# Optimization experiments

Hardware: AMD Instinct MI355X
Metric: run time of the kernel (lower is better)

## Reference

```python
import jax, jax.numpy as jnp
import numpy as np

N_HEAD = 16
NUM_GROUPS = 2


def setup_inputs() -> dict:
    key = jax.random.key(0)
    k1, k2, k3 = jax.random.split(key, 3)
    B, T, D = 4, 2048, 1024
    x = jax.random.normal(k1, (B, T, D), dtype=jnp.float32)
    W_attn = jax.random.normal(k2, (D, 3 * D), dtype=jnp.float32) * 0.02
    b_attn = jnp.zeros((3 * D,), dtype=jnp.float32)
    W_proj = jax.random.normal(k3, (D, D), dtype=jnp.float32) * 0.02
    b_proj = jnp.zeros((D,), dtype=jnp.float32)
    return {"x": x, "W_attn": W_attn, "b_attn": b_attn, "W_proj": W_proj, "b_proj": b_proj}


def _rope_tables(T, d_head):
    # thetas = 1000 ** (-2*arange(1, d/2+1)/d), repeat_interleave(2); positions start at 1
    half = d_head // 2
    thetas = 1000.0 ** (-2.0 * jnp.arange(1, half + 1, dtype=jnp.float32) / d_head)
    thetas = jnp.repeat(thetas, 2)                      # (d_head,)
    pos = jnp.arange(1, T + 1, dtype=jnp.float32)       # (T,)
    args = pos[:, None] * thetas[None, :]               # (T, d_head)
    return jnp.sin(args), jnp.cos(args)


def _apply_rope(x, sin, cos):
    # x: (B, H, T, d_head)
    x_odd = x[..., ::2]
    x_even = x[..., 1::2]
    x_sin = jnp.stack([-x_even, x_odd], axis=-1).reshape(x.shape)  # [-x1, x0, -x3, x2, ...]
    return x * cos + x_sin * sin


def reference(x, W_attn, b_attn, W_proj, b_proj):
    B, T, D = x.shape
    H = N_HEAD
    hd = D // H
    group_dim = D // NUM_GROUPS  # scale divisor; split degenerates to one group since group_dim >= hd

    qkv = x @ W_attn + b_attn                              # (B, T, 3D)
    q, k, v = jnp.split(qkv, 3, axis=-1)

    def split_heads(t):
        return t.reshape(B, T, H, hd).transpose(0, 2, 1, 3)  # (B, H, T, hd)

    q, k, v = split_heads(q), split_heads(k), split_heads(v)

    sin, cos = _rope_tables(T, hd)
    q = _apply_rope(q, sin, cos)
    k = _apply_rope(k, sin, cos)

    # NOTE: original forward never applies the causal mask (attn_mask=None) -> full softmax
    scores = jnp.einsum('bhqd,bhkd->bhqk', q, k) / jnp.sqrt(jnp.float32(group_dim))
    attn = jax.nn.softmax(scores, axis=-1)
    out = jnp.einsum('bhqk,bhkd->bhqd', attn, v)           # (B, H, T, hd)

    out = out.transpose(0, 2, 1, 3).reshape(B, T, D)       # merge heads
    return out @ W_proj + b_proj
```

## Files before the change

kernel.cpp:

```cpp
#include <hip/hip_runtime.h>
#include <hip/hip_bf16.h>
#include <stdint.h>

#define DEVI __device__ __forceinline__

using bf16x8 = __attribute__((ext_vector_type(8))) short;
using f32x4  = __attribute__((ext_vector_type(4))) float;
using f16x4  = __attribute__((ext_vector_type(4))) _Float16;
using f16x8  = __attribute__((ext_vector_type(8))) _Float16;

static constexpr int Bc = 4;
static constexpr int Tc = 2048;
static constexpr int Dc = 1024;
static constexpr int Hc = 16;
static constexpr int HDc = 64;
#define QSCALE 0.06375788883274286f

#if __has_builtin(__builtin_amdgcn_exp2f)
#define EXP2F __builtin_amdgcn_exp2f
#else
#define EXP2F exp2f
#endif

typedef const unsigned int __attribute__((address_space(1)))* gas1_t;
typedef unsigned int __attribute__((address_space(3)))* las3_t;

DEVI void gld16(const void* g, void* l)
{
    __builtin_amdgcn_global_load_lds((gas1_t)(uintptr_t)g, (las3_t)(uintptr_t)l, 16, 0, 0);
}


DEVI void transpose_tile(const float* __restrict__ W, __hip_bfloat16* __restrict__ Wt,
                         int K, int N, int n0, int k0, float (*tile)[65], int tid)
{
    const int tx = tid & 15, ty = tid >> 4;
#pragma unroll
    for (int i2 = 0; i2 < 4; i2++) {
        const int k = ty + 16 * i2;
        float4 v = *(const float4*)&W[(size_t)(k0 + k) * N + n0 + tx * 4];
        tile[tx * 4 + 0][k] = v.x;
        tile[tx * 4 + 1][k] = v.y;
        tile[tx * 4 + 2][k] = v.z;
        tile[tx * 4 + 3][k] = v.w;
    }
    __syncthreads();
#pragma unroll
    for (int i2 = 0; i2 < 4; i2++) {
        const int n = ty + 16 * i2;
        union { __hip_bfloat16 h[4]; ushort4 u4; } cv;
#pragma unroll
        for (int c = 0; c < 4; c++)
            cv.h[c] = (__hip_bfloat16)tile[n][tx * 4 + c];
        *(ushort4*)&Wt[(size_t)(n0 + n) * K + k0 + tx * 4] = cv.u4;
    }
}

__global__ __launch_bounds__(256) void prep_kernel(
    const float4* __restrict__ x, ushort4* __restrict__ xb,
    const float* __restrict__ W_attn, __hip_bfloat16* __restrict__ Wqt,
    const float* __restrict__ W_proj, __hip_bfloat16* __restrict__ Wpt,
    float* __restrict__ sinT, float* __restrict__ cosT)
{
    __shared__ float tile[64][65];
    const int bid = blockIdx.x, tid = threadIdx.x;
    if (bid < 2048) {
        const int base = bid * 1024 + tid;
#pragma unroll
        for (int u = 0; u < 4; u++) {
            const int i = base + u * 256;
            float4 v = x[i];
            union { __hip_bfloat16 h[4]; ushort4 u4; } cv;
            cv.h[0] = __float2bfloat16(v.x);
            cv.h[1] = __float2bfloat16(v.y);
            cv.h[2] = __float2bfloat16(v.z);
            cv.h[3] = __float2bfloat16(v.w);
            xb[i] = cv.u4;
        }
    } else if (bid < 2816) {
        const int b2 = bid - 2048;
        transpose_tile(W_attn, Wqt, Dc, 3 * Dc, (b2 % 48) * 64, (b2 / 48) * 64, tile, tid);
    } else if (bid < 3072) {
        const int b3 = bid - 2816;
        transpose_tile(W_proj, Wpt, Dc, Dc, (b3 % 16) * 64, (b3 / 16) * 64, tile, tid);
    } else {
        const int i = (bid - 3072) * 256 + tid;
        const int t = i >> 6, dim = i & 63;
        const int p = dim >> 1;
        float theta = powf(1000.f, -2.f * (float)(p + 1) / 64.f);
        float arg = (float)(t + 1) * theta;
        sinT[i] = sinf(arg);
        cosT[i] = cosf(arg);
    }
}


template <int MODE>
__global__ __launch_bounds__(256, 4) void gemm128(
    const __hip_bfloat16* __restrict__ A, const __hip_bfloat16* __restrict__ Bt,
    const float* __restrict__ bias, int M, int N, int K,
    const float* __restrict__ sinT, const float* __restrict__ cosT,
    __hip_bfloat16* __restrict__ Qb, __hip_bfloat16* __restrict__ Kb,
    _Float16* __restrict__ Vb, float* __restrict__ Cout)
{
    __shared__ __align__(16) __hip_bfloat16 sA[128 * 64];
    __shared__ __align__(16) __hip_bfloat16 sB[128 * 64];
    const int tid = threadIdx.x;
    const int wave = tid >> 6, lane = tid & 63;
    const int qd = lane >> 4, lm = lane & 15;
    const int wm = (wave >> 1) * 64, wn = (wave & 1) * 64;
    const int tileM = blockIdx.y * 128, tileN = blockIdx.x * 128;

    const int srow = tid >> 3;
    const int socc = (tid & 7) ^ (srow & 7);

    f32x4 acc[4][4];
#pragma unroll
    for (int i = 0; i < 4; i++)
#pragma unroll
        for (int j = 0; j < 4; j++)
            acc[i][j] = (f32x4){0.f, 0.f, 0.f, 0.f};

    const __hip_bfloat16* pa = A + (size_t)(tileM + srow) * K + socc * 8;
    const __hip_bfloat16* pb = Bt + (size_t)(tileN + srow) * K + socc * 8;

    auto stageT = [&](int k0) {
#pragma unroll
        for (int it = 0; it < 4; it++) {
            gld16(pa + (size_t)(it * 32) * K + k0, &sA[it * 2048 + wave * 512]);
            gld16(pb + (size_t)(it * 32) * K + k0, &sB[it * 2048 + wave * 512]);
        }
    };

    const int swl = (lm & 7) << 3;
    const int nk = K / 64;
    for (int kt = 0; kt < nk; kt++) {
        stageT(kt * 64);
        __builtin_amdgcn_s_waitcnt(0xF70);
        __builtin_amdgcn_s_barrier();

#pragma unroll
        for (int ks = 0; ks < 2; ks++) {
            bf16x8 wf[4], xf[4];
#pragma unroll
            for (int a = 0; a < 4; a++)
                wf[a] = *(const bf16x8*)&sB[(wn + a * 16 + lm) * 64
                                            + ((ks * 32 + qd * 8) ^ swl)];
#pragma unroll
            for (int b = 0; b < 4; b++)
                xf[b] = *(const bf16x8*)&sA[(wm + b * 16 + lm) * 64
                                            + ((ks * 32 + qd * 8) ^ swl)];
#pragma unroll
            for (int a = 0; a < 4; a++)
#pragma unroll
                for (int b = 0; b < 4; b++)
                    acc[a][b] = __builtin_amdgcn_mfma_f32_16x16x32_bf16(
                        wf[a], xf[b], acc[a][b], 0, 0, 0);
        }
        if (kt + 1 < nk)
            __builtin_amdgcn_s_barrier();
    }

    if constexpr (MODE == 0) {
        const int sec = tileN >> 10;
        const int h = ((tileN + wn) & 1023) >> 6;
#pragma unroll
        for (int a = 0; a < 4; a++) {
            const int dim0 = a * 16 + qd * 4;
            const int n0 = tileN + wn + dim0;
            const float4 bi = *(const float4*)&bias[n0];
#pragma unroll
            for (int b = 0; b < 4; b++) {
                const int m = tileM + wm + b * 16 + lm;
                const int t = m & (Tc - 1), bb = m >> 11;
                const float v0 = acc[a][b][0] + bi.x;
                const float v1 = acc[a][b][1] + bi.y;
                const float v2 = acc[a][b][2] + bi.z;
                const float v3 = acc[a][b][3] + bi.w;
                if (sec < 2) {
                    const float4 sn = *(const float4*)&sinT[t * 64 + dim0];
                    const float4 cs = *(const float4*)&cosT[t * 64 + dim0];
                    const float o0 = v0 * cs.x - v1 * sn.x;
                    const float o1 = v1 * cs.y + v0 * sn.y;
                    const float o2 = v2 * cs.z - v3 * sn.z;
                    const float o3 = v3 * cs.w + v2 * sn.w;
                    union { __hip_bfloat16 hx[4]; ushort4 u4; } cv;
                    if (sec == 0) {
                        cv.hx[0] = (__hip_bfloat16)(o0 * QSCALE);
                        cv.hx[1] = (__hip_bfloat16)(o1 * QSCALE);
                        cv.hx[2] = (__hip_bfloat16)(o2 * QSCALE);
                        cv.hx[3] = (__hip_bfloat16)(o3 * QSCALE);
                        *(ushort4*)&Qb[((size_t)(bb * Hc + h) * Tc + t) * HDc + dim0] = cv.u4;
                    } else {
                        cv.hx[0] = (__hip_bfloat16)o0;
                        cv.hx[1] = (__hip_bfloat16)o1;
                        cv.hx[2] = (__hip_bfloat16)o2;
                        cv.hx[3] = (__hip_bfloat16)o3;
                        const int dswb = dim0 ^ ((t & 7) << 3);
                        *(ushort4*)&Kb[((size_t)(bb * Hc + h) * Tc + t) * HDc + dswb] = cv.u4;
                    }
                } else {
                    const int u = t & 31;
                    const int posA = (t & ~31) + (((u & 15) >> 2) << 3)
                                     + ((u >> 4) << 2) + (u & 3);
                    const float vv[4] = {v0, v1, v2, v3};
#pragma unroll
                    for (int r = 0; r < 4; r++) {
                        const int dim = dim0 + r;
                        const int pos = posA ^ ((dim & 7) << 3);
                        Vb[((size_t)(bb * Hc + h) * HDc + dim) * Tc + pos] = (_Float16)vv[r];
                    }
                }
            }
        }
    } else {
#pragma unroll
        for (int a = 0; a < 4; a++) {
            const int n0 = tileN + wn + a * 16 + qd * 4;
            const float4 bi = *(const float4*)&bias[n0];
#pragma unroll
            for (int b = 0; b < 4; b++) {
                const int m = tileM + wm + b * 16 + lm;
                float4 o;
                o.x = acc[a][b][0] + bi.x;
                o.y = acc[a][b][1] + bi.y;
                o.z = acc[a][b][2] + bi.z;
                o.w = acc[a][b][3] + bi.w;
                *(float4*)&Cout[(size_t)m * N + n0] = o;
            }
        }
    }
}


__global__ __launch_bounds__(256, 2) void attn_kernel(
    const __hip_bfloat16* __restrict__ Qb, const __hip_bfloat16* __restrict__ Kb,
    const _Float16* __restrict__ Vh, __hip_bfloat16* __restrict__ AO)
{
    __shared__ __align__(16) __hip_bfloat16 sK[4][64 * 64];
    __shared__ __align__(16) _Float16 sV[4][64 * 64];
    const int tid = threadIdx.x, wave = tid >> 6, lane = tid & 63;
    const int qd = lane >> 4, lm = lane & 15;
    const int i = blockIdx.x;
    const int c = i & 7, j = i >> 3;
    const int bh = c + 8 * (j >> 3);
    const int qblk = j & 7;
    const int q0 = qblk * 256 + wave * 64;

    const __hip_bfloat16* Qp = Qb + (size_t)bh * Tc * HDc;
    const __hip_bfloat16* Kp = Kb + (size_t)bh * Tc * HDc;
    const _Float16* Vp = Vh + (size_t)bh * HDc * Tc;

    bf16x8 qf[4][2];
#pragma unroll
    for (int qn = 0; qn < 4; qn++)
#pragma unroll
        for (int ks = 0; ks < 2; ks++)
            qf[qn][ks] = *(const bf16x8*)(Qp + (size_t)(q0 + qn * 16 + lm) * HDc
                                          + ks * 32 + qd * 8);

    f32x4 o[4][4];
    f32x4 lsum[4];
#pragma unroll
    for (int qn = 0; qn < 4; qn++) {
#pragma unroll
        for (int cb = 0; cb < 4; cb++) o[qn][cb] = (f32x4){0.f, 0.f, 0.f, 0.f};
        lsum[qn] = (f32x4){0.f, 0.f, 0.f, 0.f};
    }
    const f16x8 one8 = {(_Float16)1.f, (_Float16)1.f, (_Float16)1.f, (_Float16)1.f,
                        (_Float16)1.f, (_Float16)1.f, (_Float16)1.f, (_Float16)1.f};

    const int swl = (lm & 7) << 3;

    auto stage = [&](int p, int k0) {
        const char* gK = (const char*)(Kp + (size_t)k0 * HDc);
#pragma unroll
        for (int jj = 0; jj < 2; jj++) {
            const int call = wave * 2 + jj;
            gld16(gK + call * 1024 + lane * 16,
                  (char*)&sK[p][0] + call * 1024 + lane * 16);
            const int dim = call * 8 + (lane >> 3);
            gld16((const char*)(Vp + (size_t)dim * Tc + k0 + (lane & 7) * 8),
                  (char*)&sV[p][0] + call * 1024 + lane * 16);
        }
    };

    constexpr int NT = Tc / 64;
    stage(0, 0);
    stage(1, 64);
    __builtin_amdgcn_s_waitcnt(0xF74);
    __builtin_amdgcn_s_barrier();

    for (int kt = 0; kt < NT; kt++) {
        const int p = kt & 3;
        if (kt + 2 < NT) stage((kt + 2) & 3, (kt + 2) * 64);

        const __hip_bfloat16* bK = &sK[p][0];
        const _Float16* bV = &sV[p][0];

        f16x8 pf8[4][2];
#pragma unroll
        for (int g = 0; g < 2; g++) {
#pragma unroll
            for (int hh = 0; hh < 2; hh++) {
                const int krow = (2 * g + hh) * 16 + lm;
                bf16x8 kf0 = *(const bf16x8*)&bK[krow * 64 + ((0 + qd * 8) ^ swl)];
                bf16x8 kf1 = *(const bf16x8*)&bK[krow * 64 + ((32 + qd * 8) ^ swl)];
#pragma unroll
                for (int qn = 0; qn < 4; qn++) {
                    f32x4 s = (f32x4){0.f, 0.f, 0.f, 0.f};
                    s = __builtin_amdgcn_mfma_f32_16x16x32_bf16(kf0, qf[qn][0], s, 0, 0, 0);
                    s = __builtin_amdgcn_mfma_f32_16x16x32_bf16(kf1, qf[qn][1], s, 0, 0, 0);
                    auto lo = __builtin_amdgcn_cvt_pkrtz(EXP2F(s[0]), EXP2F(s[1]));
                    auto hi = __builtin_amdgcn_cvt_pkrtz(EXP2F(s[2]), EXP2F(s[3]));
                    pf8[qn][g][4 * hh + 0] = lo[0];
                    pf8[qn][g][4 * hh + 1] = lo[1];
                    pf8[qn][g][4 * hh + 2] = hi[0];
                    pf8[qn][g][4 * hh + 3] = hi[1];
                }
            }
        }

#pragma unroll
        for (int qn = 0; qn < 4; qn++)
#pragma unroll
            for (int g = 0; g < 2; g++)
                lsum[qn] = __builtin_amdgcn_mfma_f32_16x16x32_f16(
                    one8, pf8[qn][g], lsum[qn], 0, 0, 0);

#pragma unroll
        for (int g = 0; g < 2; g++) {
#pragma unroll
            for (int cb = 0; cb < 4; cb++) {
                f16x8 v8 = *(const f16x8*)&bV[(cb * 16 + lm) * 64
                                              + ((g * 32 + qd * 8) ^ swl)];
#pragma unroll
                for (int qn = 0; qn < 4; qn++)
                    o[qn][cb] = __builtin_amdgcn_mfma_f32_16x16x32_f16(
                        v8, pf8[qn][g], o[qn][cb], 0, 0, 0);
            }
        }

        if (kt + 1 < NT) {
            if (kt + 2 < NT) __builtin_amdgcn_s_waitcnt(0xF74);
            else             __builtin_amdgcn_s_waitcnt(0xF70);
            __builtin_amdgcn_s_barrier();
        }
    }

    const int b = bh >> 4, h = bh & 15;
#pragma unroll
    for (int qn = 0; qn < 4; qn++) {
        const float rinv = 1.f / lsum[qn][0];
        const int t = q0 + qn * 16 + lm;
#pragma unroll
        for (int cb = 0; cb < 4; cb++)
#pragma unroll
            for (int r = 0; r < 4; r++) {
                const int dim = cb * 16 + qd * 4 + r;
                AO[((size_t)b * Tc + t) * Dc + h * HDc + dim] =
                    (__hip_bfloat16)(o[qn][cb][r] * rinv);
            }
    }
}


extern "C" void kernel_launch(void* const* d_in, const int* in_sizes, int n_in,
                              void* d_out, int out_size, void* d_ws, size_t ws_size,
                              hipStream_t stream)
{
    const float* x      = (const float*)d_in[0];
    const float* W_attn = (const float*)d_in[1];
    const float* b_attn = (const float*)d_in[2];
    const float* W_proj = (const float*)d_in[3];
    const float* b_proj = (const float*)d_in[4];
    float* out = (float*)d_out;

    char* w = (char*)d_ws;
    auto alloc = [&](size_t bytes) -> char* {
        char* p = w;
        w += (bytes + 255) & ~(size_t)255;
        return p;
    };
    __hip_bfloat16* xb  = (__hip_bfloat16*)alloc((size_t)Bc * Tc * Dc * 2);
    __hip_bfloat16* Wqt = (__hip_bfloat16*)alloc((size_t)3 * Dc * Dc * 2);
    __hip_bfloat16* Wpt = (__hip_bfloat16*)alloc((size_t)Dc * Dc * 2);
    __hip_bfloat16* Qb  = (__hip_bfloat16*)alloc((size_t)Bc * Hc * Tc * HDc * 2);
    __hip_bfloat16* Kb  = (__hip_bfloat16*)alloc((size_t)Bc * Hc * Tc * HDc * 2);
    _Float16*       Vh  = (_Float16*)alloc((size_t)Bc * Hc * Tc * HDc * 2);
    __hip_bfloat16* AO  = (__hip_bfloat16*)alloc((size_t)Bc * Tc * Dc * 2);
    float* sinT = (float*)alloc((size_t)Tc * 64 * 4);
    float* cosT = (float*)alloc((size_t)Tc * 64 * 4);

    const int M = Bc * Tc;

    prep_kernel<<<dim3(3584), dim3(256), 0, stream>>>(
        (const float4*)x, (ushort4*)xb, W_attn, Wqt, W_proj, Wpt, sinT, cosT);

    gemm128<0><<<dim3(3 * Dc / 128, M / 128), dim3(256), 0, stream>>>(
        xb, Wqt, b_attn, M, 3 * Dc, Dc, sinT, cosT, Qb, Kb, Vh, nullptr);

    attn_kernel<<<dim3(512), dim3(256), 0, stream>>>(Qb, Kb, Vh, AO);

    gemm128<1><<<dim3(Dc / 128, M / 128), dim3(256), 0, stream>>>(
        AO, Wpt, b_proj, M, Dc, Dc, nullptr, nullptr, nullptr, nullptr, nullptr, out);
}
```

Measured before the change: 260.1 us.

## Software-pipeline QK^T of next key tile with PV of current tile

Restructures the attention inner loop so the QK^T MFMAs and exp2 for tile kt+1 are issued alongside the P·V MFMAs for tile kt. Ping-pong P-fragment buffers and a two-way unrolled loop carry this across iterations. The LDS prefetch depth grows from two to three tiles in flight over the existing four buffers, with the waitcnt adjusted to match. The aim is to hide exp and LDS latency behind matrix work, at the cost of many more live VGPRs (a full 4x4 score array plus two P buffers), which may cut occupancy or cause spills.

```diff
diff --git a/kernel.cpp b/kernel.cpp
--- a/kernel.cpp
+++ b/kernel.cpp
@@ -285,51 +285,68 @@
         }
     };
 
+    auto qk_into = [&](const __hip_bfloat16* bK, f32x4 (&s)[4][4]) {
+#pragma unroll
+        for (int nb = 0; nb < 4; nb++) {
+            const int krow = nb * 16 + lm;
+            bf16x8 kf0 = *(const bf16x8*)&bK[krow * 64 + ((0 + qd * 8) ^ swl)];
+            bf16x8 kf1 = *(const bf16x8*)&bK[krow * 64 + ((32 + qd * 8) ^ swl)];
+#pragma unroll
+            for (int qn = 0; qn < 4; qn++) {
+                f32x4 t = (f32x4){0.f, 0.f, 0.f, 0.f};
+                t = __builtin_amdgcn_mfma_f32_16x16x32_bf16(kf0, qf[qn][0], t, 0, 0, 0);
+                t = __builtin_amdgcn_mfma_f32_16x16x32_bf16(kf1, qf[qn][1], t, 0, 0, 0);
+                s[qn][nb] = t;
+            }
+        }
+    };
+
+    auto exp_into = [&](const f32x4 (&s)[4][4], int g, f16x8 (&pf)[4][2]) {
+#pragma unroll
+        for (int qn = 0; qn < 4; qn++) {
+            const f32x4 a = s[qn][2 * g], b2 = s[qn][2 * g + 1];
+            auto l0 = __builtin_amdgcn_cvt_pkrtz(EXP2F(a[0]), EXP2F(a[1]));
+            auto l1 = __builtin_amdgcn_cvt_pkrtz(EXP2F(a[2]), EXP2F(a[3]));
+            auto h0 = __builtin_amdgcn_cvt_pkrtz(EXP2F(b2[0]), EXP2F(b2[1]));
+            auto h1 = __builtin_amdgcn_cvt_pkrtz(EXP2F(b2[2]), EXP2F(b2[3]));
+            pf[qn][g][0] = l0[0]; pf[qn][g][1] = l0[1];
+            pf[qn][g][2] = l1[0]; pf[qn][g][3] = l1[1];
+            pf[qn][g][4] = h0[0]; pf[qn][g][5] = h0[1];
+            pf[qn][g][6] = h1[0]; pf[qn][g][7] = h1[1];
+        }
+    };
+
     constexpr int NT = Tc / 64;
     stage(0, 0);
     stage(1, 64);
+    stage(2, 128);
     __builtin_amdgcn_s_waitcnt(0xF74);
     __builtin_amdgcn_s_barrier();
 
-    for (int kt = 0; kt < NT; kt++) {
+    f16x8 pfA[4][2], pfB[4][2];
+    {
+        f32x4 s0[4][4];
+        qk_into(&sK[0][0], s0);
+#pragma unroll
+        for (int g = 0; g < 2; g++) exp_into(s0, g, pfA);
+    }
+
+    auto body = [&](int kt, f16x8 (&pfC)[4][2], f16x8 (&pfN)[4][2]) {
         const int p = kt & 3;
-        if (kt + 2 < NT) stage((kt + 2) & 3, (kt + 2) * 64);
-
-        const __hip_bfloat16* bK = &sK[p][0];
+        if (kt + 3 < NT) stage((kt + 3) & 3, (kt + 3) * 64);
+
+        f32x4 s[4][4];
+        const bool hasN = (kt + 1 < NT);
+        if (hasN) qk_into(&sK[(kt + 1) & 3][0], s);
+
         const _Float16* bV = &sV[p][0];
-
-        f16x8 pf8[4][2];
 #pragma unroll
         for (int g = 0; g < 2; g++) {
-#pragma unroll
-            for (int hh = 0; hh < 2; hh++) {
-                const int krow = (2 * g + hh) * 16 + lm;
-                bf16x8 kf0 = *(const bf16x8*)&bK[krow * 64 + ((0 + qd * 8) ^ swl)];
-                bf16x8 kf1 = *(const bf16x8*)&bK[krow * 64 + ((32 + qd * 8) ^ swl)];
-#pragma unroll
-                for (int qn = 0; qn < 4; qn++) {
-                    f32x4 s = (f32x4){0.f, 0.f, 0.f, 0.f};
-                    s = __builtin_amdgcn_mfma_f32_16x16x32_bf16(kf0, qf[qn][0], s, 0, 0, 0);
-                    s = __builtin_amdgcn_mfma_f32_16x16x32_bf16(kf1, qf[qn][1], s, 0, 0, 0);
-                    auto lo = __builtin_amdgcn_cvt_pkrtz(EXP2F(s[0]), EXP2F(s[1]));
-                    auto hi = __builtin_amdgcn_cvt_pkrtz(EXP2F(s[2]), EXP2F(s[3]));
-                    pf8[qn][g][4 * hh + 0] = lo[0];
-                    pf8[qn][g][4 * hh + 1] = lo[1];
-                    pf8[qn][g][4 * hh + 2] = hi[0];
-                    pf8[qn][g][4 * hh + 3] = hi[1];
-                }
-            }
-        }
-
-#pragma unroll
-        for (int qn = 0; qn < 4; qn++)
-#pragma unroll
-            for (int g = 0; g < 2; g++)
+            if (hasN) exp_into(s, g, pfN);
+#pragma unroll
+            for (int qn = 0; qn < 4; qn++)
                 lsum[qn] = __builtin_amdgcn_mfma_f32_16x16x32_f16(
-                    one8, pf8[qn][g], lsum[qn], 0, 0, 0);
-
-#pragma unroll
-        for (int g = 0; g < 2; g++) {
+                    one8, pfC[qn][g], lsum[qn], 0, 0, 0);
 #pragma unroll
             for (int cb = 0; cb < 4; cb++) {
                 f16x8 v8 = *(const f16x8*)&bV[(cb * 16 + lm) * 64
@@ -337,15 +354,20 @@
 #pragma unroll
                 for (int qn = 0; qn < 4; qn++)
                     o[qn][cb] = __builtin_amdgcn_mfma_f32_16x16x32_f16(
-                        v8, pf8[qn][g], o[qn][cb], 0, 0, 0);
+                        v8, pfC[qn][g], o[qn][cb], 0, 0, 0);
             }
         }
 
         if (kt + 1 < NT) {
-            if (kt + 2 < NT) __builtin_amdgcn_s_waitcnt(0xF74);
+            if (kt + 3 < NT) __builtin_amdgcn_s_waitcnt(0xF74);
             else             __builtin_amdgcn_s_waitcnt(0xF70);
             __builtin_amdgcn_s_barrier();
         }
+    };
+
+    for (int kt = 0; kt < NT; kt += 2) {
+        body(kt, pfA, pfB);
+        body(kt + 1, pfB, pfA);
     }
 
     const int b = bh >> 4, h = bh & 15;
```

New measurement: 338.6 us. 30.2% more time.
